# Performance work log

Measured on AMD Instinct MI355X. Metric: run time of the kernel, lower is better.

The kernel has to match this reference:

```python
import jax, jax.numpy as jnp
import numpy as np

HEADS = 4
KS = 7  # neighborhood window size


def group_norm(x, g, b, eps=1e-5):
    # GroupNorm(1, C) on NCHW: normalize over (C,H,W) per sample
    mu = x.mean(axis=(1, 2, 3), keepdims=True)
    var = x.var(axis=(1, 2, 3), keepdims=True)
    xn = (x - mu) * jax.lax.rsqrt(var + eps)
    return xn * g[None, :, None, None] + b[None, :, None, None]


def layer_norm(x, g, b, eps=1e-5):
    mu = x.mean(axis=-1, keepdims=True)
    var = x.var(axis=-1, keepdims=True)
    return (x - mu) * jax.lax.rsqrt(var + eps) * g + b


def na2d(x, qkv_w, qkv_b, proj_w, proj_b, rpb):
    # Neighborhood attention 2D (NATTEN semantics: window clamped at borders)
    N, H, W, C = x.shape
    e, k = HEADS, KS
    d = C // e
    qkv = x @ qkv_w.T + qkv_b  # [N,H,W,3C]
    q, kk, v = jnp.split(qkv, 3, axis=-1)
    q = q.reshape(N, H, W, e, d) * (d ** -0.5)
    kk = kk.reshape(N, H, W, e, d)
    v = v.reshape(N, H, W, e, d)
    ni = jnp.clip(jnp.arange(H) - k // 2, 0, H - k)[:, None] + jnp.arange(k)  # [H,k]
    nj = jnp.clip(jnp.arange(W) - k // 2, 0, W - k)[:, None] + jnp.arange(k)  # [W,k]
    kg = kk[:, ni][:, :, :, nj]  # [N,H,i,W,j,e,d]
    vg = v[:, ni][:, :, :, nj]
    scores = jnp.einsum('nhwed,nhiwjed->nhweij', q, kg)  # [N,H,W,e,k,k]
    ri = ni - jnp.arange(H)[:, None] + (k - 1)  # rel pos index in [0, 2k-2]
    rj = nj - jnp.arange(W)[:, None] + (k - 1)
    bias = rpb[:, ri][:, :, :, rj]  # [e,H,i,W,j]
    scores = scores + bias.transpose(1, 3, 0, 2, 4)[None]
    attn = jax.nn.softmax(scores.reshape(N, H, W, e, k * k), axis=-1).reshape(N, H, W, e, k, k)
    out = jnp.einsum('nhweij,nhiwjed->nhwed', attn, vg).reshape(N, H, W, C)
    return out @ proj_w.T + proj_b


def na_layer(x, gn_g, gn_b, qkv_w, qkv_b, proj_w, proj_b, rpb, ln_g, ln_b, fc1_w, fc1_b, fc2_w, fc2_b):
    N, C, H, W = x.shape
    x1 = x.transpose(0, 2, 3, 1)  # n h w c (pre-norm residual)
    xg = group_norm(x, gn_g, gn_b).transpose(0, 2, 3, 1)
    a = na2d(xg, qkv_w, qkv_b, proj_w, proj_b, rpb) + x1
    t = a.reshape(N, H * W, C)
    h = jax.nn.gelu(layer_norm(t, ln_g, ln_b) @ fc1_w.T + fc1_b, approximate=False)
    t = t + (h @ fc2_w.T + fc2_b)
    return t.reshape(N, H, W, C).transpose(0, 3, 1, 2)


def conv3x3(x, w, b):
    y = jax.lax.conv_general_dilated(x, w, (1, 1), 'SAME', dimension_numbers=('NCHW', 'OIHW', 'NCHW'))
    return y + b[None, :, None, None]


def setup_inputs() -> dict:
    key = jax.random.key(0)
    ks = jax.random.split(key, 16)
    N, C, H, W = 2, 128, 64, 64
    L, e, k, hid, red = 2, HEADS, KS, 4 * 128, 18
    rn = lambda kk, shape, s=0.02: jax.random.normal(kk, shape, jnp.float32) * s
    return {
        'x': jax.random.normal(ks[0], (N, C, H, W), jnp.float32),
        'gn_g': jnp.ones((L, C), jnp.float32), 'gn_b': jnp.zeros((L, C), jnp.float32),
        'qkv_w': rn(ks[1], (L, 3 * C, C)), 'qkv_b': jnp.zeros((L, 3 * C), jnp.float32),
        'proj_w': rn(ks[2], (L, C, C)), 'proj_b': jnp.zeros((L, C), jnp.float32),
        'rpb': rn(ks[3], (L, e, 2 * k - 1, 2 * k - 1)),
        'ln_g': jnp.ones((L, C), jnp.float32), 'ln_b': jnp.zeros((L, C), jnp.float32),
        'fc1_w': rn(ks[4], (L, hid, C)), 'fc1_b': jnp.zeros((L, hid), jnp.float32),
        'fc2_w': rn(ks[5], (L, C, hid)), 'fc2_b': jnp.zeros((L, C), jnp.float32),
        'bconv_w': rn(ks[6], (C, C, 3, 3)), 'bconv_b': jnp.zeros((C,), jnp.float32),
        'c1_w': rn(ks[7], (C // 4, C)), 'c1_b': jnp.zeros((C // 4,), jnp.float32),
        'c2_w': rn(ks[8], (C, C // 4)), 'c2_b': jnp.zeros((C,), jnp.float32),
        'ca1_w': rn(ks[9], (C // red, C)), 'ca1_b': jnp.zeros((C // red,), jnp.float32),
        'ca2_w': rn(ks[10], (C, C // red)), 'ca2_b': jnp.zeros((C,), jnp.float32),
    }


def reference(x, gn_g, gn_b, qkv_w, qkv_b, proj_w, proj_b, rpb, ln_g, ln_b, fc1_w, fc1_b, fc2_w, fc2_b, bconv_w, bconv_b, c1_w, c1_b, c2_w, c2_b, ca1_w, ca1_b, ca2_w, ca2_b):
    res = x
    for l in range(gn_g.shape[0]):  # n_resblocks (structurally fixed, small)
        res = na_layer(res, gn_g[l], gn_b[l], qkv_w[l], qkv_b[l], proj_w[l], proj_b[l], rpb[l],
                       ln_g[l], ln_b[l], fc1_w[l], fc1_b[l], fc2_w[l], fc2_b[l])
    res = conv3x3(res, bconv_w, bconv_b)
    # tail: 1x1 conv -> ReLU -> 1x1 conv -> CALayer
    y = jax.nn.relu(jnp.einsum('rc,nchw->nrhw', c1_w, res) + c1_b[None, :, None, None])
    y = jnp.einsum('cr,nrhw->nchw', c2_w, y) + c2_b[None, :, None, None]
    p = y.mean(axis=(2, 3))  # global avg pool -> [N,C]
    s = jax.nn.sigmoid(jax.nn.relu(p @ ca1_w.T + ca1_b) @ ca2_w.T + ca2_b)
    y = y * s[:, :, None, None]
    return y + x
```

## Files before the change

### kernel.cpp

```cpp
#include <hip/hip_runtime.h>
#include <math.h>

typedef unsigned short u16;

#define NN 2
#define CC 128
#define HH 64
#define WW 64
#define NHD 4
#define DH 32
#define KSZ 7
#define PIX (NN*HH*WW)
#define HID 512
#define C4 32
#define CRED 7
#define RW 22
#define RNB 160
#define NBV 154

typedef float f32x4 __attribute__((ext_vector_type(4)));
typedef short bf16x8 __attribute__((ext_vector_type(8)));

static __device__ __forceinline__ float u2f(u16 u){ return __uint_as_float(((unsigned)u) << 16); }
static __device__ __forceinline__ u16 f2u(float f){
    unsigned b = __float_as_uint(f);
    return (u16)((b + 0x7FFFu + ((b >> 16) & 1u)) >> 16);
}

__global__ void detect_k(const u16* __restrict__ x, int* __restrict__ flag,
                         float* __restrict__ poolacc){
    __shared__ float red[256];
    int t = threadIdx.x;
    float mx = 0.f;
    for(int i = t; i < 4096; i += 256){
        float v = fabsf(u2f(x[i]));
        if(v < 1e30f) mx = fmaxf(mx, v);
    }
    red[t] = mx; __syncthreads();
    for(int s = 128; s > 0; s >>= 1){
        if(t < s) red[t] = fmaxf(red[t], red[t+s]);
        __syncthreads();
    }
    if(t == 0) *flag = (red[0] > 1e6f) ? 1 : 0;
    if(t < NN*CC) poolacc[t] = 0.f;
}

struct PtrTab { const void* p[23]; int off[24]; };
#define NCVT 2172
#define NRPK 576
#define NNCH 512

__global__ __launch_bounds__(256) void setup_k(
    PtrTab tab, u16* __restrict__ Wb, u16* __restrict__ Wt,
    const void* __restrict__ convw, const void* __restrict__ x,
    float* __restrict__ cur, float* __restrict__ part,
    const int* __restrict__ flag, int total)
{
    int blk = blockIdx.x;
    int t = threadIdx.x;
    int fl = *flag;
    if(blk < NCVT){
        int i = blk*256 + t;
        if(i < total){
            int a = 0;
            while(i >= tab.off[a+1]) a++;
            int loc = i - tab.off[a];
            Wb[i] = fl ? f2u(((const float*)tab.p[a])[loc]) : ((const u16*)tab.p[a])[loc];
        }
        return;
    }
    if(blk < NCVT + NRPK){
        int i = (blk - NCVT)*256 + t;
        if(i < CC*CC*9){
            int o = i/(9*CC); int rem = i%(9*CC); int tap = rem/CC; int c = rem%CC;
            size_t s = (size_t)(o*CC + c)*9 + tap;
            Wt[i] = fl ? f2u(((const float*)convw)[s]) : ((const u16*)convw)[s];
        }
        return;
    }
    __shared__ float tile[32][65];
    __shared__ float wred[4][2];
    int u = blk - NCVT - NRPK;
    int bx = u & 3, by = u >> 2;
    int n = by >> 6, i = by & 63;
    for(int idx = t; idx < 32*64; idx += 256){
        int cl = idx >> 6, j = idx & 63;
        size_t src = ((size_t)(n*CC + bx*32 + cl)*HH + i)*WW + j;
        tile[cl][j] = fl ? ((const float*)x)[src] : u2f(((const u16*)x)[src]);
    }
    __syncthreads();
    float s = 0.f, q = 0.f;
    for(int idx = t; idx < 64*32; idx += 256){
        int j = idx >> 5, cl = idx & 31;
        float v = tile[cl][j];
        cur[((size_t)((n*HH + i)*WW) + j)*CC + bx*32 + cl] = v;
        s += v; q += v*v;
    }
    #pragma unroll
    for(int off = 32; off > 0; off >>= 1){ s += __shfl_xor(s, off, 64); q += __shfl_xor(q, off, 64); }
    int wave = t >> 6;
    if((t & 63) == 0){ wred[wave][0] = s; wred[wave][1] = q; }
    __syncthreads();
    if(t == 0){
        float ss = wred[0][0]+wred[1][0]+wred[2][0]+wred[3][0];
        float qq = wred[0][1]+wred[1][1]+wred[2][1]+wred[3][1];
        int pidx = n*256 + i*4 + bx;
        part[pidx*2] = ss; part[pidx*2+1] = qq;
    }
}

enum { EPI_NONE = 0, EPI_RES = 1, EPI_GELU = 2 };
enum { OUT_F32 = 0, OUT_BF16 = 1, OUT_BOTH = 2 };
enum { EX_NONE = 0, EX_STATS = 1 };
#define LDP 136

template<int EPI, int OUTM, int AGN, int EXTRA>
__global__ __launch_bounds__(256) void g64_k(
    const void* __restrict__ Av, const u16* __restrict__ W, const u16* __restrict__ bias,
    const float* __restrict__ R, float* __restrict__ Cf, u16* __restrict__ Cb,
    const u16* __restrict__ gnw, const u16* __restrict__ gnb,
    float* __restrict__ gnpart, int gncount,
    int M, int N, int K)
{
    __shared__ __align__(16) u16 As[64*LDP];
    __shared__ __align__(16) u16 Bs[64*LDP];
    __shared__ float wred[4][2];
    const int bm = blockIdx.y*64, bn = blockIdx.x*64;
    const int t = threadIdx.x;
    const int wave = t >> 6, lane = t & 63;
    const int wm = (wave >> 1)*32, wn = (wave & 1)*32;
    const int lg = lane >> 4, lr = lane & 15;
    const int nsm = bm >> 12;
    f32x4 acc[2][2];
    #pragma unroll
    for(int i = 0; i < 2; i++)
        #pragma unroll
        for(int j = 0; j < 2; j++) acc[i][j] = (f32x4){0.f,0.f,0.f,0.f};

    float gmu = 0.f, grs = 0.f;
    if(AGN){
        float a = 0.f, q = 0.f;
        for(int idx = lane; idx < gncount; idx += 64){
            a += gnpart[(nsm*gncount + idx)*2];
            q += gnpart[(nsm*gncount + idx)*2 + 1];
        }
        #pragma unroll
        for(int off = 32; off > 0; off >>= 1){
            a += __shfl_xor(a, off, 64); q += __shfl_xor(q, off, 64);
        }
        const float inv = 1.f/(float)(HH*WW*CC);
        gmu = a*inv;
        grs = rsqrtf(fmaxf(q*inv - gmu*gmu, 0.f) + 1e-5f);
    }

    for(int k0 = 0; k0 < K; k0 += 128){
        uint4 ra[4], rb[4];
        float4 fa[4][2];
        #pragma unroll
        for(int r = 0; r < 4; r++){
            int e = r*256 + t;
            int row = e >> 4, ch = e & 15;
            if(AGN){
                const float* ap = (const float*)Av + (size_t)(bm+row)*K + k0 + ch*8;
                fa[r][0] = *(const float4*)ap;
                fa[r][1] = *(const float4*)(ap + 4);
            } else {
                ra[r] = *(const uint4*)((const u16*)Av + (size_t)(bm+row)*K + k0 + ch*8);
            }
            rb[r] = (bn+row < N) ? *(const uint4*)(W + (size_t)(bn+row)*K + k0 + ch*8)
                                 : (uint4){0,0,0,0};
        }
        #pragma unroll
        for(int r = 0; r < 4; r++){
            int e = r*256 + t;
            int row = e >> 4, ch = e & 15;
            if(AGN){
                union { uint4 u; u16 h[8]; } g8, b8, o8;
                g8.u = *(const uint4*)(gnw + k0 + ch*8);
                b8.u = *(const uint4*)(gnb + k0 + ch*8);
                const float* fv = (const float*)&fa[r][0];
                #pragma unroll
                for(int z = 0; z < 8; z++)
                    o8.h[z] = f2u((fv[z]-gmu)*grs*u2f(g8.h[z]) + u2f(b8.h[z]));
                *(uint4*)&As[row*LDP + ch*8] = o8.u;
            } else {
                *(uint4*)&As[row*LDP + ch*8] = ra[r];
            }
            *(uint4*)&Bs[row*LDP + ch*8] = rb[r];
        }
        __syncthreads();
        #pragma unroll
        for(int kc = 0; kc < 4; kc++){
            bf16x8 af0 = *(const bf16x8*)&As[(wm + lr)*LDP      + kc*32 + lg*8];
            bf16x8 af1 = *(const bf16x8*)&As[(wm + 16 + lr)*LDP + kc*32 + lg*8];
            bf16x8 bf0 = *(const bf16x8*)&Bs[(wn + lr)*LDP      + kc*32 + lg*8];
            bf16x8 bf1 = *(const bf16x8*)&Bs[(wn + 16 + lr)*LDP + kc*32 + lg*8];
            acc[0][0] = __builtin_amdgcn_mfma_f32_16x16x32_bf16(af0, bf0, acc[0][0], 0, 0, 0);
            acc[0][1] = __builtin_amdgcn_mfma_f32_16x16x32_bf16(af0, bf1, acc[0][1], 0, 0, 0);
            acc[1][0] = __builtin_amdgcn_mfma_f32_16x16x32_bf16(af1, bf0, acc[1][0], 0, 0, 0);
            acc[1][1] = __builtin_amdgcn_mfma_f32_16x16x32_bf16(af1, bf1, acc[1][1], 0, 0, 0);
        }
        if(k0 + 128 < K) __syncthreads();
    }

    float ssum = 0.f, sq = 0.f;
    #pragma unroll
    for(int i = 0; i < 2; i++){
        #pragma unroll
        for(int j = 0; j < 2; j++){
            int col = bn + wn + j*16 + lr;
            if(col >= N) continue;
            #pragma unroll
            for(int reg = 0; reg < 4; reg++){
                int row = bm + wm + i*16 + lg*4 + reg;
                float v = acc[i][j][reg] + u2f(bias[col]);
                if(EPI == EPI_RES)  v += R[(size_t)row*N + col];
                if(EPI == EPI_GELU) v = 0.5f*v*(1.f + erff(v*0.70710678118f));
                if(OUTM == OUT_F32 || OUTM == OUT_BOTH) Cf[(size_t)row*N + col] = v;
                if(OUTM == OUT_BF16 || OUTM == OUT_BOTH) Cb[(size_t)row*N + col] = f2u(v);
                if(EXTRA == EX_STATS){ ssum += v; sq += v*v; }
            }
        }
    }
    if(EXTRA == EX_STATS){
        #pragma unroll
        for(int off = 32; off > 0; off >>= 1){
            ssum += __shfl_xor(ssum, off, 64); sq += __shfl_xor(sq, off, 64);
        }
        if(lane == 0){ wred[wave][0] = ssum; wred[wave][1] = sq; }
        __syncthreads();
        if(t == 0){
            int bidx = blockIdx.y*gridDim.x + blockIdx.x;
            gnpart[bidx*2]   = wred[0][0]+wred[1][0]+wred[2][0]+wred[3][0];
            gnpart[bidx*2+1] = wred[0][1]+wred[1][1]+wred[2][1]+wred[3][1];
        }
    }
}

__global__ __launch_bounds__(256) void proj_ln_k(
    const u16* __restrict__ A, const u16* __restrict__ W, const u16* __restrict__ bias,
    const float* __restrict__ R, const u16* __restrict__ lng, const u16* __restrict__ lnb,
    float* __restrict__ abuf, u16* __restrict__ lnout)
{
    __shared__ __align__(16) u16 As[64*LDP];
    __shared__ __align__(16) u16 Bs[128*LDP];
    __shared__ float redS[64][2], redQ[64][2], muS[64], rsS[64];
    const int bm = blockIdx.x*64;
    const int t = threadIdx.x;
    const int wave = t >> 6, lane = t & 63;
    const int wm = (wave >> 1)*32, wn = (wave & 1)*64;
    const int lg = lane >> 4, lr = lane & 15;

    {
        uint4 ra[4], rb[8];
        #pragma unroll
        for(int r = 0; r < 4; r++){
            int e = r*256 + t; int row = e >> 4, ch = e & 15;
            ra[r] = *(const uint4*)(A + (size_t)(bm+row)*CC + ch*8);
        }
        #pragma unroll
        for(int r = 0; r < 8; r++){
            int e = r*256 + t; int row = e >> 4, ch = e & 15;
            rb[r] = *(const uint4*)(W + (size_t)row*CC + ch*8);
        }
        #pragma unroll
        for(int r = 0; r < 4; r++){
            int e = r*256 + t; int row = e >> 4, ch = e & 15;
            *(uint4*)&As[row*LDP + ch*8] = ra[r];
        }
        #pragma unroll
        for(int r = 0; r < 8; r++){
            int e = r*256 + t; int row = e >> 4, ch = e & 15;
            *(uint4*)&Bs[row*LDP + ch*8] = rb[r];
        }
    }
    __syncthreads();

    f32x4 acc[2][4];
    #pragma unroll
    for(int i = 0; i < 2; i++)
        #pragma unroll
        for(int j = 0; j < 4; j++) acc[i][j] = (f32x4){0.f,0.f,0.f,0.f};
    #pragma unroll
    for(int kc = 0; kc < 4; kc++){
        bf16x8 af[2], bf[4];
        #pragma unroll
        for(int i = 0; i < 2; i++)
            af[i] = *(const bf16x8*)&As[(wm + i*16 + lr)*LDP + kc*32 + lg*8];
        #pragma unroll
        for(int j = 0; j < 4; j++)
            bf[j] = *(const bf16x8*)&Bs[(wn + j*16 + lr)*LDP + kc*32 + lg*8];
        #pragma unroll
        for(int i = 0; i < 2; i++)
            #pragma unroll
            for(int j = 0; j < 4; j++)
                acc[i][j] = __builtin_amdgcn_mfma_f32_16x16x32_bf16(af[i], bf[j], acc[i][j], 0, 0, 0);
    }
    #pragma unroll
    for(int i = 0; i < 2; i++){
        #pragma unroll
        for(int reg = 0; reg < 4; reg++){
            int rl = wm + i*16 + lg*4 + reg;
            float rs_ = 0.f, rq_ = 0.f;
            #pragma unroll
            for(int j = 0; j < 4; j++){
                int col = wn + j*16 + lr;
                float v = acc[i][j][reg] + u2f(bias[col]) + R[(size_t)(bm+rl)*CC + col];
                acc[i][j][reg] = v;
                abuf[(size_t)(bm+rl)*CC + col] = v;
                rs_ += v; rq_ += v*v;
            }
            rs_ += __shfl_xor(rs_, 1, 64); rq_ += __shfl_xor(rq_, 1, 64);
            rs_ += __shfl_xor(rs_, 2, 64); rq_ += __shfl_xor(rq_, 2, 64);
            rs_ += __shfl_xor(rs_, 4, 64); rq_ += __shfl_xor(rq_, 4, 64);
            rs_ += __shfl_xor(rs_, 8, 64); rq_ += __shfl_xor(rq_, 8, 64);
            if(lr == 0){ redS[rl][wn>>6] = rs_; redQ[rl][wn>>6] = rq_; }
        }
    }
    __syncthreads();
    if(t < 64){
        float mu = (redS[t][0] + redS[t][1])*(1.f/CC);
        float var = fmaxf((redQ[t][0] + redQ[t][1])*(1.f/CC) - mu*mu, 0.f);
        muS[t] = mu; rsS[t] = rsqrtf(var + 1e-5f);
    }
    __syncthreads();
    #pragma unroll
    for(int i = 0; i < 2; i++){
        #pragma unroll
        for(int reg = 0; reg < 4; reg++){
            int rl = wm + i*16 + lg*4 + reg;
            float mu = muS[rl], rstd = rsS[rl];
            #pragma unroll
            for(int j = 0; j < 4; j++){
                int col = wn + j*16 + lr;
                float v = (acc[i][j][reg] - mu)*rstd*u2f(lng[col]) + u2f(lnb[col]);
                lnout[(size_t)(bm+rl)*CC + col] = f2u(v);
            }
        }
    }
}

__global__ __launch_bounds__(256) void mconv_k(
    const u16* __restrict__ in, const u16* __restrict__ Wt,
    const u16* __restrict__ bias, u16* __restrict__ Cb)
{
    __shared__ __align__(16) u16 As[64*LDP];
    __shared__ __align__(16) u16 Bs[64*LDP];
    const int bm = blockIdx.y*64, bn = blockIdx.x*64;
    const int t = threadIdx.x;
    const int wave = t >> 6, lane = t & 63;
    const int wm = (wave >> 1)*32, wn = (wave & 1)*32;
    const int lg = lane >> 4, lr = lane & 15;
    f32x4 acc[2][2];
    #pragma unroll
    for(int i = 0; i < 2; i++)
        #pragma unroll
        for(int j = 0; j < 2; j++) acc[i][j] = (f32x4){0.f,0.f,0.f,0.f};

    for(int tap = 0; tap < 9; tap++){
        int dy = tap/3 - 1, dx = tap%3 - 1;
        int k0 = tap*128;
        uint4 ra[4], rb[4];
        #pragma unroll
        for(int r = 0; r < 4; r++){
            int e = r*256 + t;
            int row = e >> 4, ch = e & 15;
            int p = bm + row;
            int n = p >> 12, ii = (p & 4095) >> 6, jj = p & 63;
            int y = ii + dy, x = jj + dx;
            ra[r] = (uint4){0,0,0,0};
            if(y >= 0 && y < HH && x >= 0 && x < WW)
                ra[r] = *(const uint4*)(in + (size_t)(((n*HH + y)*WW + x))*CC + ch*8);
            rb[r] = *(const uint4*)(Wt + (size_t)(bn+row)*(9*CC) + k0 + ch*8);
        }
        #pragma unroll
        for(int r = 0; r < 4; r++){
            int e = r*256 + t;
            int row = e >> 4, ch = e & 15;
            *(uint4*)&As[row*LDP + ch*8] = ra[r];
            *(uint4*)&Bs[row*LDP + ch*8] = rb[r];
        }
        __syncthreads();
        #pragma unroll
        for(int kc = 0; kc < 4; kc++){
            bf16x8 af0 = *(const bf16x8*)&As[(wm + lr)*LDP      + kc*32 + lg*8];
            bf16x8 af1 = *(const bf16x8*)&As[(wm + 16 + lr)*LDP + kc*32 + lg*8];
            bf16x8 bf0 = *(const bf16x8*)&Bs[(wn + lr)*LDP      + kc*32 + lg*8];
            bf16x8 bf1 = *(const bf16x8*)&Bs[(wn + 16 + lr)*LDP + kc*32 + lg*8];
            acc[0][0] = __builtin_amdgcn_mfma_f32_16x16x32_bf16(af0, bf0, acc[0][0], 0, 0, 0);
            acc[0][1] = __builtin_amdgcn_mfma_f32_16x16x32_bf16(af0, bf1, acc[0][1], 0, 0, 0);
            acc[1][0] = __builtin_amdgcn_mfma_f32_16x16x32_bf16(af1, bf0, acc[1][0], 0, 0, 0);
            acc[1][1] = __builtin_amdgcn_mfma_f32_16x16x32_bf16(af1, bf1, acc[1][1], 0, 0, 0);
        }
        if(tap < 8) __syncthreads();
    }
    #pragma unroll
    for(int i = 0; i < 2; i++){
        #pragma unroll
        for(int j = 0; j < 2; j++){
            int col = bn + wn + j*16 + lr;
            #pragma unroll
            for(int reg = 0; reg < 4; reg++){
                int row = bm + wm + i*16 + lg*4 + reg;
                Cb[(size_t)row*CC + col] = f2u(acc[i][j][reg] + u2f(bias[col]));
            }
        }
    }
}

#define KVP 72
#define PSP 168

__global__ __launch_bounds__(128) void att_tile_k(
    const u16* __restrict__ qkv, const u16* __restrict__ rpb, u16* __restrict__ out)
{
    __shared__ __align__(16) u16 KV[2][RNB][KVP];
    __shared__ __align__(16) u16 Qs[16][64];
    __shared__ __align__(16) u16 Ps[2][16][PSP];
    __shared__ float rpbs[2][169];
    const int blk = blockIdx.x;
    const int rb = blk >> 1, eg = blk & 1;
    const int p0 = rb*16;
    const int jb = p0 & 63, i = (p0 >> 6) & 63, n = p0 >> 12;
    const int i0 = min(max(i-3, 0), HH-KSZ);
    const int rc0 = min(max(jb-3, 0), WW-KSZ);
    const int t = threadIdx.x;

    for(int idx = t; idx < 2*169; idx += 128)
        rpbs[idx/169][idx%169] = u2f(rpb[(eg*2 + idx/169)*169 + idx%169]);
    {
        int pix = t >> 3, ch = t & 7;
        *(uint4*)&Qs[pix][ch*8] = *(const uint4*)(qkv + (size_t)(p0+pix)*(3*CC) + eg*64 + ch*8);
    }
    for(int idx = t; idx < RNB*16; idx += 128){
        int nb = idx >> 4, part = idx & 15;
        int kv = part >> 3, ch = part & 7;
        uint4 v = (uint4){0,0,0,0};
        if(nb < NBV){
            int ky = nb/RW, kcol = nb - ky*RW;
            int sy = i0 + ky, sx = min(rc0 + kcol, WW-1);
            v = *(const uint4*)(qkv + (size_t)((n*HH + sy)*WW + sx)*(3*CC) + CC + kv*CC + eg*64 + ch*8);
        }
        *(uint4*)&KV[kv][nb][ch*8] = v;
    }
    __syncthreads();

    const int el = t >> 6;
    const int lane = t & 63, lg = lane >> 4, lr = lane & 15;

    bf16x8 aq = *(const bf16x8*)&Qs[lr][el*32 + lg*8];
    f32x4 sc[10];
    #pragma unroll
    for(int c = 0; c < 10; c++){
        bf16x8 bk = *(const bf16x8*)&KV[0][c*16+lr][el*32 + lg*8];
        sc[c] = __builtin_amdgcn_mfma_f32_16x16x32_bf16(aq, bk, (f32x4){0.f,0.f,0.f,0.f}, 0, 0, 0);
    }
    #pragma unroll
    for(int reg = 0; reg < 4; reg++){
        int pix = lg*4 + reg;
        int j = jb + pix;
        int base = min(max(j-3, 0), WW-KSZ) - rc0;
        float mx = -1e30f;
        #pragma unroll
        for(int c = 0; c < 10; c++){
            int nb = c*16 + lr;
            int ky = nb/RW, kcol = nb - ky*RW;
            float v = -1e30f;
            if(nb < NBV && kcol >= base && kcol <= base+6){
                int ri = i0 + ky - i + (KSZ-1);
                int rj = rc0 + kcol - j + (KSZ-1);
                v = sc[c][reg]*0.17677669529663689f + rpbs[el][ri*13 + rj];
            }
            sc[c][reg] = v;
            mx = fmaxf(mx, v);
        }
        mx = fmaxf(mx, __shfl_xor(mx, 1, 64));
        mx = fmaxf(mx, __shfl_xor(mx, 2, 64));
        mx = fmaxf(mx, __shfl_xor(mx, 4, 64));
        mx = fmaxf(mx, __shfl_xor(mx, 8, 64));
        float sum = 0.f;
        #pragma unroll
        for(int c = 0; c < 10; c++){
            float p = __expf(sc[c][reg] - mx);
            sc[c][reg] = p; sum += p;
        }
        sum += __shfl_xor(sum, 1, 64);
        sum += __shfl_xor(sum, 2, 64);
        sum += __shfl_xor(sum, 4, 64);
        sum += __shfl_xor(sum, 8, 64);
        float rs = 1.f/sum;
        #pragma unroll
        for(int c = 0; c < 10; c++)
            Ps[el][pix][c*16+lr] = f2u(sc[c][reg]*rs);
    }
    __syncthreads();
    f32x4 o0 = (f32x4){0.f,0.f,0.f,0.f}, o1 = (f32x4){0.f,0.f,0.f,0.f};
    #pragma unroll
    for(int ks = 0; ks < 5; ks++){
        bf16x8 ap = *(const bf16x8*)&Ps[el][lr][ks*32 + lg*8];
        bf16x8 b0, b1;
        #pragma unroll
        for(int jj = 0; jj < 8; jj++){
            int nb = ks*32 + lg*8 + jj;
            b0[jj] = (short)KV[1][nb][el*32 + lr];
            b1[jj] = (short)KV[1][nb][el*32 + 16 + lr];
        }
        o0 = __builtin_amdgcn_mfma_f32_16x16x32_bf16(ap, b0, o0, 0, 0, 0);
        o1 = __builtin_amdgcn_mfma_f32_16x16x32_bf16(ap, b1, o1, 0, 0, 0);
    }
    int e = eg*2 + el;
    #pragma unroll
    for(int reg = 0; reg < 4; reg++){
        int pix = lg*4 + reg;
        out[(size_t)(p0+pix)*CC + e*32 + lr]      = f2u(o0[reg]);
        out[(size_t)(p0+pix)*CC + e*32 + 16 + lr] = f2u(o1[reg]);
    }
}

__global__ __launch_bounds__(256) void tail_k(
    const u16* __restrict__ A, const u16* __restrict__ c1w, const u16* __restrict__ c1b,
    const u16* __restrict__ c2w, const u16* __restrict__ c2b,
    float* __restrict__ ybuf, float* __restrict__ poolacc)
{
    __shared__ __align__(16) u16 As[64*LDP];
    __shared__ __align__(16) u16 Bs1[32*LDP];
    __shared__ __align__(16) u16 Hs[64*40];
    __shared__ __align__(16) u16 Bs2[128*40];
    const int bm = blockIdx.x*64;
    const int t = threadIdx.x;
    const int wave = t >> 6, lane = t & 63;
    const int lg = lane >> 4, lr = lane & 15;
    const int nsm = bm >> 12;

    {
        uint4 ra[4], rb1[2], rb2[2];
        #pragma unroll
        for(int r = 0; r < 4; r++){
            int e = r*256 + t; int row = e >> 4, ch = e & 15;
            ra[r] = *(const uint4*)(A + (size_t)(bm+row)*CC + ch*8);
        }
        #pragma unroll
        for(int r = 0; r < 2; r++){
            int e = r*256 + t; int row = e >> 4, ch = e & 15;
            rb1[r] = *(const uint4*)(c1w + (size_t)row*CC + ch*8);
        }
        #pragma unroll
        for(int r = 0; r < 2; r++){
            int e = r*256 + t; int row = e >> 2, ch = e & 3;
            rb2[r] = *(const uint4*)(c2w + (size_t)row*C4 + ch*8);
        }
        #pragma unroll
        for(int r = 0; r < 4; r++){
            int e = r*256 + t; int row = e >> 4, ch = e & 15;
            *(uint4*)&As[row*LDP + ch*8] = ra[r];
        }
        #pragma unroll
        for(int r = 0; r < 2; r++){
            int e = r*256 + t; int row = e >> 4, ch = e & 15;
            *(uint4*)&Bs1[row*LDP + ch*8] = rb1[r];
        }
        #pragma unroll
        for(int r = 0; r < 2; r++){
            int e = r*256 + t; int row = e >> 2, ch = e & 3;
            *(uint4*)&Bs2[row*40 + ch*8] = rb2[r];
        }
    }
    __syncthreads();

    {
        const int wm1 = (wave >> 1)*32, wn1 = (wave & 1)*16;
        f32x4 a1[2];
        a1[0] = (f32x4){0.f,0.f,0.f,0.f}; a1[1] = (f32x4){0.f,0.f,0.f,0.f};
        #pragma unroll
        for(int kc = 0; kc < 4; kc++){
            bf16x8 bf = *(const bf16x8*)&Bs1[(wn1 + lr)*LDP + kc*32 + lg*8];
            bf16x8 af0 = *(const bf16x8*)&As[(wm1 + lr)*LDP      + kc*32 + lg*8];
            bf16x8 af1 = *(const bf16x8*)&As[(wm1 + 16 + lr)*LDP + kc*32 + lg*8];
            a1[0] = __builtin_amdgcn_mfma_f32_16x16x32_bf16(af0, bf, a1[0], 0, 0, 0);
            a1[1] = __builtin_amdgcn_mfma_f32_16x16x32_bf16(af1, bf, a1[1], 0, 0, 0);
        }
        #pragma unroll
        for(int i = 0; i < 2; i++){
            #pragma unroll
            for(int reg = 0; reg < 4; reg++){
                int rl = wm1 + i*16 + lg*4 + reg;
                int col = wn1 + lr;
                Hs[rl*40 + col] = f2u(fmaxf(a1[i][reg] + u2f(c1b[col]), 0.f));
            }
        }
    }
    __syncthreads();

    {
        const int wm = (wave >> 1)*32, wn = (wave & 1)*64;
        f32x4 a2[2][4];
        #pragma unroll
        for(int i = 0; i < 2; i++)
            #pragma unroll
            for(int j = 0; j < 4; j++) a2[i][j] = (f32x4){0.f,0.f,0.f,0.f};
        bf16x8 af[2];
        #pragma unroll
        for(int i = 0; i < 2; i++)
            af[i] = *(const bf16x8*)&Hs[(wm + i*16 + lr)*40 + lg*8];
        #pragma unroll
        for(int j = 0; j < 4; j++){
            bf16x8 bf = *(const bf16x8*)&Bs2[(wn + j*16 + lr)*40 + lg*8];
            a2[0][j] = __builtin_amdgcn_mfma_f32_16x16x32_bf16(af[0], bf, a2[0][j], 0, 0, 0);
            a2[1][j] = __builtin_amdgcn_mfma_f32_16x16x32_bf16(af[1], bf, a2[1][j], 0, 0, 0);
        }
        float cs[4] = {0.f,0.f,0.f,0.f};
        #pragma unroll
        for(int i = 0; i < 2; i++){
            #pragma unroll
            for(int j = 0; j < 4; j++){
                int col = wn + j*16 + lr;
                #pragma unroll
                for(int reg = 0; reg < 4; reg++){
                    int row = bm + wm + i*16 + lg*4 + reg;
                    float v = a2[i][j][reg] + u2f(c2b[col]);
                    ybuf[(size_t)row*CC + col] = v;
                    cs[j] += v;
                }
            }
        }
        #pragma unroll
        for(int j = 0; j < 4; j++){
            cs[j] += __shfl_xor(cs[j], 16, 64);
            cs[j] += __shfl_xor(cs[j], 32, 64);
        }
        if(lg == 0){
            #pragma unroll
            for(int j = 0; j < 4; j++)
                atomicAdd(&poolacc[nsm*CC + wn + j*16 + lr], cs[j]);
        }
    }
}

__global__ __launch_bounds__(256) void final_ca_k(
    const float* __restrict__ y, const float* __restrict__ poolacc,
    const u16* __restrict__ w1, const u16* __restrict__ b1,
    const u16* __restrict__ w2, const u16* __restrict__ b2,
    const void* __restrict__ xraw, void* __restrict__ outv,
    const int* __restrict__ flag)
{
    __shared__ float t1s[CRED];
    __shared__ float sres;
    int id0 = blockIdx.x*256;
    int c = (id0 >> 12) & (CC-1);
    int n = id0 >> 19;
    int t = threadIdx.x;
    if(t < CRED){
        float a = u2f(b1[t]);
        const float pscale = 1.f/(float)(HH*WW);
        for(int cc = 0; cc < CC; cc++)
            a += poolacc[n*CC + cc]*pscale*u2f(w1[t*CC + cc]);
        t1s[t] = fmaxf(a, 0.f);
    }
    __syncthreads();
    if(t == 0){
        float a = u2f(b2[c]);
        #pragma unroll
        for(int r = 0; r < CRED; r++) a += t1s[r]*u2f(w2[c*CRED + r]);
        sres = 1.f/(1.f + __expf(-a));
    }
    __syncthreads();
    float s = sres;
    int id = id0 + t;
    int j = id & 63; int i = (id >> 6) & 63;
    float xr = (*flag) ? ((const float*)xraw)[id] : u2f(((const u16*)xraw)[id]);
    float v = y[(size_t)((n*HH + i)*WW + j)*CC + c]*s + xr;
    if(*flag) ((float*)outv)[id] = v;
    else      ((u16*)outv)[id] = f2u(v);
}

extern "C" void kernel_launch(void* const* d_in, const int* in_sizes, int n_in,
                              void* d_out, int out_size, void* d_ws, size_t ws_size,
                              hipStream_t stream){
    float* wsf    = (float*)d_ws;
    int*   flagp  = (int*)d_ws;
    float* gnpart = wsf + 8;
    float* poolacc= wsf + 1040;

    u16* Wb = (u16*)(wsf + 2048);
    static const int wsizes[23] = {256,256,98304,768,32768,256,1352,256,256,131072,1024,
                                   131072,256,147456,128,4096,32,4096,128,896,7,896,128};
    int woff[24]; woff[0] = 0;
    for(int i = 0; i < 23; i++) woff[i+1] = woff[i] + wsizes[i];
    const int WTOT = woff[23];
    u16* Wt = Wb + 555760;

    float* AB    = wsf + 360448;
    float* cur   = AB;
    u16*  cur16  = (u16*)(AB + 1048576);
    u16*  xg16   = (u16*)(AB + 1572864);
    u16*  qkv16  = (u16*)(AB + 2097152);
    float* abuf  = AB + 2097152;
    u16*  hbuf16 = (u16*)(AB + 3670016);
    float* ybuf  = AB + 3670016;

    detect_k<<<1, 256, 0, stream>>>((const u16*)d_in[0], flagp, poolacc);

    PtrTab tab;
    for(int i = 0; i < 23; i++){ tab.p[i] = d_in[i+1]; tab.off[i] = woff[i]; }
    tab.off[23] = woff[23];
    setup_k<<<NCVT + NRPK + NNCH, 256, 0, stream>>>(
        tab, Wb, Wt, d_in[14], d_in[0], cur, gnpart, flagp, WTOT);

    const u16 *gng = Wb+woff[0], *gnb = Wb+woff[1], *qkvw = Wb+woff[2], *qkvb = Wb+woff[3],
              *projw = Wb+woff[4], *projb = Wb+woff[5], *rpbw = Wb+woff[6], *lng = Wb+woff[7],
              *lnb = Wb+woff[8], *f1w = Wb+woff[9], *f1b = Wb+woff[10], *f2w = Wb+woff[11],
              *f2b = Wb+woff[12], *bcb = Wb+woff[14], *c1w = Wb+woff[15],
              *c1b = Wb+woff[16], *c2w = Wb+woff[17], *c2b = Wb+woff[18], *ca1w = Wb+woff[19],
              *ca1b = Wb+woff[20], *ca2w = Wb+woff[21], *ca2b = Wb+woff[22];

    for(int l = 0; l < 2; l++){
        int gncount = (l == 0) ? 256 : 128;

        g64_k<EPI_NONE,OUT_BF16,1,EX_NONE><<<dim3(6, PIX/64), 256, 0, stream>>>(
            cur, qkvw + (size_t)l*3*CC*CC, qkvb + l*3*CC, nullptr, nullptr, qkv16,
            gng + l*CC, gnb + l*CC, gnpart, gncount, PIX, 3*CC, CC);

        att_tile_k<<<PIX/16*2, 128, 0, stream>>>(qkv16, rpbw + l*NHD*169, xg16);

        proj_ln_k<<<PIX/64, 256, 0, stream>>>(
            xg16, projw + (size_t)l*CC*CC, projb + l*CC, cur, lng + l*CC, lnb + l*CC,
            abuf, xg16);

        g64_k<EPI_GELU,OUT_BF16,0,EX_NONE><<<dim3(8, PIX/64), 256, 0, stream>>>(
            xg16, f1w + (size_t)l*HID*CC, f1b + l*HID, nullptr, nullptr, hbuf16,
            nullptr, nullptr, nullptr, 0, PIX, HID, CC);

        g64_k<EPI_RES,OUT_BOTH,0,EX_STATS><<<dim3(2, PIX/64), 256, 0, stream>>>(
            hbuf16, f2w + (size_t)l*CC*HID, f2b + l*CC, abuf, cur, cur16,
            nullptr, nullptr, gnpart, 0, PIX, CC, HID);
    }

    mconv_k<<<dim3(2, PIX/64), 256, 0, stream>>>(cur16, Wt, bcb, xg16);

    tail_k<<<PIX/64, 256, 0, stream>>>(xg16, c1w, c1b, c2w, c2b, ybuf, poolacc);

    final_ca_k<<<(NN*CC*HH*WW)/256, 256, 0, stream>>>(
        ybuf, poolacc, ca1w, ca1b, ca2w, ca2b, d_in[0], d_out, flagp);
}
```

Before: 268.9 us.

## Fuse 3x3 conv with tail 1x1 convs and shrink proj_ln tiles to 32 rows

```diff
diff --git a/kernel.cpp b/kernel.cpp
--- a/kernel.cpp
+++ b/kernel.cpp
@@ -242,19 +242,19 @@
     const float* __restrict__ R, const u16* __restrict__ lng, const u16* __restrict__ lnb,
     float* __restrict__ abuf, u16* __restrict__ lnout)
 {
-    __shared__ __align__(16) u16 As[64*LDP];
+    __shared__ __align__(16) u16 As[32*LDP];
     __shared__ __align__(16) u16 Bs[128*LDP];
-    __shared__ float redS[64][2], redQ[64][2], muS[64], rsS[64];
-    const int bm = blockIdx.x*64;
+    __shared__ float redS[32][2], redQ[32][2], muS[32], rsS[32];
+    const int bm = blockIdx.x*32;
     const int t = threadIdx.x;
     const int wave = t >> 6, lane = t & 63;
-    const int wm = (wave >> 1)*32, wn = (wave & 1)*64;
+    const int wm = (wave >> 1)*16, wn = (wave & 1)*64;
     const int lg = lane >> 4, lr = lane & 15;
 
     {
-        uint4 ra[4], rb[8];
-        #pragma unroll
-        for(int r = 0; r < 4; r++){
+        uint4 ra[2], rb[8];
+        #pragma unroll
+        for(int r = 0; r < 2; r++){
             int e = r*256 + t; int row = e >> 4, ch = e & 15;
             ra[r] = *(const uint4*)(A + (size_t)(bm+row)*CC + ch*8);
         }
@@ -264,7 +264,7 @@
             rb[r] = *(const uint4*)(W + (size_t)row*CC + ch*8);
         }
         #pragma unroll
-        for(int r = 0; r < 4; r++){
+        for(int r = 0; r < 2; r++){
             int e = r*256 + t; int row = e >> 4, ch = e & 15;
             *(uint4*)&As[row*LDP + ch*8] = ra[r];
         }
@@ -276,134 +276,201 @@
     }
     __syncthreads();
 
-    f32x4 acc[2][4];
-    #pragma unroll
-    for(int i = 0; i < 2; i++)
-        #pragma unroll
-        for(int j = 0; j < 4; j++) acc[i][j] = (f32x4){0.f,0.f,0.f,0.f};
+    f32x4 acc[4];
+    #pragma unroll
+    for(int j = 0; j < 4; j++) acc[j] = (f32x4){0.f,0.f,0.f,0.f};
     #pragma unroll
     for(int kc = 0; kc < 4; kc++){
-        bf16x8 af[2], bf[4];
-        #pragma unroll
-        for(int i = 0; i < 2; i++)
-            af[i] = *(const bf16x8*)&As[(wm + i*16 + lr)*LDP + kc*32 + lg*8];
-        #pragma unroll
-        for(int j = 0; j < 4; j++)
-            bf[j] = *(const bf16x8*)&Bs[(wn + j*16 + lr)*LDP + kc*32 + lg*8];
-        #pragma unroll
-        for(int i = 0; i < 2; i++)
-            #pragma unroll
-            for(int j = 0; j < 4; j++)
-                acc[i][j] = __builtin_amdgcn_mfma_f32_16x16x32_bf16(af[i], bf[j], acc[i][j], 0, 0, 0);
-    }
-    #pragma unroll
-    for(int i = 0; i < 2; i++){
-        #pragma unroll
-        for(int reg = 0; reg < 4; reg++){
-            int rl = wm + i*16 + lg*4 + reg;
-            float rs_ = 0.f, rq_ = 0.f;
-            #pragma unroll
-            for(int j = 0; j < 4; j++){
-                int col = wn + j*16 + lr;
-                float v = acc[i][j][reg] + u2f(bias[col]) + R[(size_t)(bm+rl)*CC + col];
-                acc[i][j][reg] = v;
-                abuf[(size_t)(bm+rl)*CC + col] = v;
-                rs_ += v; rq_ += v*v;
-            }
-            rs_ += __shfl_xor(rs_, 1, 64); rq_ += __shfl_xor(rq_, 1, 64);
-            rs_ += __shfl_xor(rs_, 2, 64); rq_ += __shfl_xor(rq_, 2, 64);
-            rs_ += __shfl_xor(rs_, 4, 64); rq_ += __shfl_xor(rq_, 4, 64);
-            rs_ += __shfl_xor(rs_, 8, 64); rq_ += __shfl_xor(rq_, 8, 64);
-            if(lr == 0){ redS[rl][wn>>6] = rs_; redQ[rl][wn>>6] = rq_; }
-        }
-    }
-    __syncthreads();
-    if(t < 64){
+        bf16x8 af = *(const bf16x8*)&As[(wm + lr)*LDP + kc*32 + lg*8];
+        #pragma unroll
+        for(int j = 0; j < 4; j++){
+            bf16x8 bf = *(const bf16x8*)&Bs[(wn + j*16 + lr)*LDP + kc*32 + lg*8];
+            acc[j] = __builtin_amdgcn_mfma_f32_16x16x32_bf16(af, bf, acc[j], 0, 0, 0);
+        }
+    }
+    #pragma unroll
+    for(int reg = 0; reg < 4; reg++){
+        int rl = wm + lg*4 + reg;
+        float rs_ = 0.f, rq_ = 0.f;
+        #pragma unroll
+        for(int j = 0; j < 4; j++){
+            int col = wn + j*16 + lr;
+            float v = acc[j][reg] + u2f(bias[col]) + R[(size_t)(bm+rl)*CC + col];
+            acc[j][reg] = v;
+            abuf[(size_t)(bm+rl)*CC + col] = v;
+            rs_ += v; rq_ += v*v;
+        }
+        rs_ += __shfl_xor(rs_, 1, 64); rq_ += __shfl_xor(rq_, 1, 64);
+        rs_ += __shfl_xor(rs_, 2, 64); rq_ += __shfl_xor(rq_, 2, 64);
+        rs_ += __shfl_xor(rs_, 4, 64); rq_ += __shfl_xor(rq_, 4, 64);
+        rs_ += __shfl_xor(rs_, 8, 64); rq_ += __shfl_xor(rq_, 8, 64);
+        if(lr == 0){ redS[rl][wn>>6] = rs_; redQ[rl][wn>>6] = rq_; }
+    }
+    __syncthreads();
+    if(t < 32){
         float mu = (redS[t][0] + redS[t][1])*(1.f/CC);
         float var = fmaxf((redQ[t][0] + redQ[t][1])*(1.f/CC) - mu*mu, 0.f);
         muS[t] = mu; rsS[t] = rsqrtf(var + 1e-5f);
     }
     __syncthreads();
     #pragma unroll
-    for(int i = 0; i < 2; i++){
-        #pragma unroll
-        for(int reg = 0; reg < 4; reg++){
-            int rl = wm + i*16 + lg*4 + reg;
-            float mu = muS[rl], rstd = rsS[rl];
-            #pragma unroll
-            for(int j = 0; j < 4; j++){
-                int col = wn + j*16 + lr;
-                float v = (acc[i][j][reg] - mu)*rstd*u2f(lng[col]) + u2f(lnb[col]);
-                lnout[(size_t)(bm+rl)*CC + col] = f2u(v);
-            }
-        }
-    }
-}
-
-__global__ __launch_bounds__(256) void mconv_k(
-    const u16* __restrict__ in, const u16* __restrict__ Wt,
-    const u16* __restrict__ bias, u16* __restrict__ Cb)
+    for(int reg = 0; reg < 4; reg++){
+        int rl = wm + lg*4 + reg;
+        float mu = muS[rl], rstd = rsS[rl];
+        #pragma unroll
+        for(int j = 0; j < 4; j++){
+            int col = wn + j*16 + lr;
+            float v = (acc[j][reg] - mu)*rstd*u2f(lng[col]) + u2f(lnb[col]);
+            lnout[(size_t)(bm+rl)*CC + col] = f2u(v);
+        }
+    }
+}
+
+__global__ __launch_bounds__(256) void mct_k(
+    const u16* __restrict__ in, const u16* __restrict__ Wt, const u16* __restrict__ bias,
+    const u16* __restrict__ c1w, const u16* __restrict__ c1b,
+    const u16* __restrict__ c2w, const u16* __restrict__ c2b,
+    float* __restrict__ ybuf, float* __restrict__ poolacc)
 {
-    __shared__ __align__(16) u16 As[64*LDP];
-    __shared__ __align__(16) u16 Bs[64*LDP];
-    const int bm = blockIdx.y*64, bn = blockIdx.x*64;
+    __shared__ __align__(16) u16 As[32*LDP];
+    __shared__ __align__(16) u16 Bs[128*LDP];
+    u16* Bs1 = Bs;
+    u16* Bs2 = Bs + 32*LDP;
+    u16* Hs  = Bs + 32*LDP + 128*40;
+    const int bm = blockIdx.x*32;
     const int t = threadIdx.x;
     const int wave = t >> 6, lane = t & 63;
-    const int wm = (wave >> 1)*32, wn = (wave & 1)*32;
+    const int wm = (wave >> 1)*16, wn = (wave & 1)*64;
     const int lg = lane >> 4, lr = lane & 15;
-    f32x4 acc[2][2];
-    #pragma unroll
-    for(int i = 0; i < 2; i++)
-        #pragma unroll
-        for(int j = 0; j < 2; j++) acc[i][j] = (f32x4){0.f,0.f,0.f,0.f};
+    const int nsm = bm >> 12;
+
+    uint4 rb1[2], rb2[2];
+    #pragma unroll
+    for(int r = 0; r < 2; r++){
+        int e = r*256 + t; int row = e >> 4, ch = e & 15;
+        rb1[r] = *(const uint4*)(c1w + (size_t)row*CC + ch*8);
+    }
+    #pragma unroll
+    for(int r = 0; r < 2; r++){
+        int e = r*256 + t; int row = e >> 2, ch = e & 3;
+        rb2[r] = *(const uint4*)(c2w + (size_t)row*C4 + ch*8);
+    }
+
+    f32x4 acc[4];
+    #pragma unroll
+    for(int j = 0; j < 4; j++) acc[j] = (f32x4){0.f,0.f,0.f,0.f};
 
     for(int tap = 0; tap < 9; tap++){
         int dy = tap/3 - 1, dx = tap%3 - 1;
-        int k0 = tap*128;
-        uint4 ra[4], rb[4];
-        #pragma unroll
-        for(int r = 0; r < 4; r++){
-            int e = r*256 + t;
-            int row = e >> 4, ch = e & 15;
+        uint4 ra[2], rb[8];
+        #pragma unroll
+        for(int r = 0; r < 2; r++){
+            int e = r*256 + t; int row = e >> 4, ch = e & 15;
             int p = bm + row;
             int n = p >> 12, ii = (p & 4095) >> 6, jj = p & 63;
             int y = ii + dy, x = jj + dx;
             ra[r] = (uint4){0,0,0,0};
             if(y >= 0 && y < HH && x >= 0 && x < WW)
                 ra[r] = *(const uint4*)(in + (size_t)(((n*HH + y)*WW + x))*CC + ch*8);
-            rb[r] = *(const uint4*)(Wt + (size_t)(bn+row)*(9*CC) + k0 + ch*8);
-        }
-        #pragma unroll
-        for(int r = 0; r < 4; r++){
-            int e = r*256 + t;
-            int row = e >> 4, ch = e & 15;
+        }
+        #pragma unroll
+        for(int r = 0; r < 8; r++){
+            int e = r*256 + t; int row = e >> 4, ch = e & 15;
+            rb[r] = *(const uint4*)(Wt + (size_t)row*(9*CC) + tap*128 + ch*8);
+        }
+        #pragma unroll
+        for(int r = 0; r < 2; r++){
+            int e = r*256 + t; int row = e >> 4, ch = e & 15;
             *(uint4*)&As[row*LDP + ch*8] = ra[r];
+        }
+        #pragma unroll
+        for(int r = 0; r < 8; r++){
+            int e = r*256 + t; int row = e >> 4, ch = e & 15;
             *(uint4*)&Bs[row*LDP + ch*8] = rb[r];
         }
         __syncthreads();
         #pragma unroll
         for(int kc = 0; kc < 4; kc++){
-            bf16x8 af0 = *(const bf16x8*)&As[(wm + lr)*LDP      + kc*32 + lg*8];
-            bf16x8 af1 = *(const bf16x8*)&As[(wm + 16 + lr)*LDP + kc*32 + lg*8];
-            bf16x8 bf0 = *(const bf16x8*)&Bs[(wn + lr)*LDP      + kc*32 + lg*8];
-            bf16x8 bf1 = *(const bf16x8*)&Bs[(wn + 16 + lr)*LDP + kc*32 + lg*8];
-            acc[0][0] = __builtin_amdgcn_mfma_f32_16x16x32_bf16(af0, bf0, acc[0][0], 0, 0, 0);
-            acc[0][1] = __builtin_amdgcn_mfma_f32_16x16x32_bf16(af0, bf1, acc[0][1], 0, 0, 0);
-            acc[1][0] = __builtin_amdgcn_mfma_f32_16x16x32_bf16(af1, bf0, acc[1][0], 0, 0, 0);
-            acc[1][1] = __builtin_amdgcn_mfma_f32_16x16x32_bf16(af1, bf1, acc[1][1], 0, 0, 0);
-        }
-        if(tap < 8) __syncthreads();
-    }
-    #pragma unroll
-    for(int i = 0; i < 2; i++){
-        #pragma unroll
-        for(int j = 0; j < 2; j++){
-            int col = bn + wn + j*16 + lr;
+            bf16x8 af = *(const bf16x8*)&As[(wm + lr)*LDP + kc*32 + lg*8];
+            #pragma unroll
+            for(int j = 0; j < 4; j++){
+                bf16x8 bf = *(const bf16x8*)&Bs[(wn + j*16 + lr)*LDP + kc*32 + lg*8];
+                acc[j] = __builtin_amdgcn_mfma_f32_16x16x32_bf16(af, bf, acc[j], 0, 0, 0);
+            }
+        }
+        __syncthreads();
+    }
+
+    #pragma unroll
+    for(int j = 0; j < 4; j++){
+        int col = wn + j*16 + lr;
+        #pragma unroll
+        for(int reg = 0; reg < 4; reg++){
+            int rl = wm + lg*4 + reg;
+            As[rl*LDP + col] = f2u(acc[j][reg] + u2f(bias[col]));
+        }
+    }
+    #pragma unroll
+    for(int r = 0; r < 2; r++){
+        int e = r*256 + t; int row = e >> 4, ch = e & 15;
+        *(uint4*)&Bs1[row*LDP + ch*8] = rb1[r];
+    }
+    #pragma unroll
+    for(int r = 0; r < 2; r++){
+        int e = r*256 + t; int row = e >> 2, ch = e & 3;
+        *(uint4*)&Bs2[row*40 + ch*8] = rb2[r];
+    }
+    __syncthreads();
+
+    {
+        const int wn1 = (wave & 1)*16;
+        f32x4 a1 = (f32x4){0.f,0.f,0.f,0.f};
+        #pragma unroll
+        for(int kc = 0; kc < 4; kc++){
+            bf16x8 af = *(const bf16x8*)&As[(wm + lr)*LDP + kc*32 + lg*8];
+            bf16x8 bf = *(const bf16x8*)&Bs1[(wn1 + lr)*LDP + kc*32 + lg*8];
+            a1 = __builtin_amdgcn_mfma_f32_16x16x32_bf16(af, bf, a1, 0, 0, 0);
+        }
+        #pragma unroll
+        for(int reg = 0; reg < 4; reg++){
+            int rl = wm + lg*4 + reg;
+            int col = wn1 + lr;
+            Hs[rl*40 + col] = f2u(fmaxf(a1[reg] + u2f(c1b[col]), 0.f));
+        }
+    }
+    __syncthreads();
+
+    {
+        f32x4 a2[4];
+        #pragma unroll
+        for(int j = 0; j < 4; j++) a2[j] = (f32x4){0.f,0.f,0.f,0.f};
+        bf16x8 af = *(const bf16x8*)&Hs[(wm + lr)*40 + lg*8];
+        #pragma unroll
+        for(int j = 0; j < 4; j++){
+            bf16x8 bf = *(const bf16x8*)&Bs2[(wn + j*16 + lr)*40 + lg*8];
+            a2[j] = __builtin_amdgcn_mfma_f32_16x16x32_bf16(af, bf, a2[j], 0, 0, 0);
+        }
+        float cs[4] = {0.f,0.f,0.f,0.f};
+        #pragma unroll
+        for(int j = 0; j < 4; j++){
+            int col = wn + j*16 + lr;
             #pragma unroll
             for(int reg = 0; reg < 4; reg++){
-                int row = bm + wm + i*16 + lg*4 + reg;
-                Cb[(size_t)row*CC + col] = f2u(acc[i][j][reg] + u2f(bias[col]));
+                int row = bm + wm + lg*4 + reg;
+                float v = a2[j][reg] + u2f(c2b[col]);
+                ybuf[(size_t)row*CC + col] = v;
+                cs[j] += v;
             }
+        }
+        #pragma unroll
+        for(int j = 0; j < 4; j++){
+            cs[j] += __shfl_xor(cs[j], 16, 64);
+            cs[j] += __shfl_xor(cs[j], 32, 64);
+        }
+        if(lg == 0){
+            #pragma unroll
+            for(int j = 0; j < 4; j++)
+                atomicAdd(&poolacc[nsm*CC + wn + j*16 + lr], cs[j]);
         }
     }
 }
@@ -416,8 +483,8 @@
 {
     __shared__ __align__(16) u16 KV[2][RNB][KVP];
     __shared__ __align__(16) u16 Qs[16][64];
-    __shared__ __align__(16) u16 Ps[2][16][PSP];
     __shared__ float rpbs[2][169];
+    u16* PsB = &KV[0][0][0];
     const int blk = blockIdx.x;
     const int rb = blk >> 1, eg = blk & 1;
     const int p0 = rb*16;
@@ -455,6 +522,7 @@
         bf16x8 bk = *(const bf16x8*)&KV[0][c*16+lr][el*32 + lg*8];
         sc[c] = __builtin_amdgcn_mfma_f32_16x16x32_bf16(aq, bk, (f32x4){0.f,0.f,0.f,0.f}, 0, 0, 0);
     }
+    __syncthreads();
     #pragma unroll
     for(int reg = 0; reg < 4; reg++){
         int pix = lg*4 + reg;
@@ -491,13 +559,13 @@
         float rs = 1.f/sum;
         #pragma unroll
         for(int c = 0; c < 10; c++)
-            Ps[el][pix][c*16+lr] = f2u(sc[c][reg]*rs);
+            PsB[(el*16 + pix)*PSP + c*16 + lr] = f2u(sc[c][reg]*rs);
     }
     __syncthreads();
     f32x4 o0 = (f32x4){0.f,0.f,0.f,0.f}, o1 = (f32x4){0.f,0.f,0.f,0.f};
     #pragma unroll
     for(int ks = 0; ks < 5; ks++){
-        bf16x8 ap = *(const bf16x8*)&Ps[el][lr][ks*32 + lg*8];
+        bf16x8 ap = *(const bf16x8*)&PsB[(el*16 + lr)*PSP + ks*32 + lg*8];
         bf16x8 b0, b1;
         #pragma unroll
         for(int jj = 0; jj < 8; jj++){
@@ -514,125 +582,6 @@
         int pix = lg*4 + reg;
         out[(size_t)(p0+pix)*CC + e*32 + lr]      = f2u(o0[reg]);
         out[(size_t)(p0+pix)*CC + e*32 + 16 + lr] = f2u(o1[reg]);
-    }
-}
-
-__global__ __launch_bounds__(256) void tail_k(
-    const u16* __restrict__ A, const u16* __restrict__ c1w, const u16* __restrict__ c1b,
-    const u16* __restrict__ c2w, const u16* __restrict__ c2b,
-    float* __restrict__ ybuf, float* __restrict__ poolacc)
-{
-    __shared__ __align__(16) u16 As[64*LDP];
-    __shared__ __align__(16) u16 Bs1[32*LDP];
-    __shared__ __align__(16) u16 Hs[64*40];
-    __shared__ __align__(16) u16 Bs2[128*40];
-    const int bm = blockIdx.x*64;
-    const int t = threadIdx.x;
-    const int wave = t >> 6, lane = t & 63;
-    const int lg = lane >> 4, lr = lane & 15;
-    const int nsm = bm >> 12;
-
-    {
-        uint4 ra[4], rb1[2], rb2[2];
-        #pragma unroll
-        for(int r = 0; r < 4; r++){
-            int e = r*256 + t; int row = e >> 4, ch = e & 15;
-            ra[r] = *(const uint4*)(A + (size_t)(bm+row)*CC + ch*8);
-        }
-        #pragma unroll
-        for(int r = 0; r < 2; r++){
-            int e = r*256 + t; int row = e >> 4, ch = e & 15;
-            rb1[r] = *(const uint4*)(c1w + (size_t)row*CC + ch*8);
-        }
-        #pragma unroll
-        for(int r = 0; r < 2; r++){
-            int e = r*256 + t; int row = e >> 2, ch = e & 3;
-            rb2[r] = *(const uint4*)(c2w + (size_t)row*C4 + ch*8);
-        }
-        #pragma unroll
-        for(int r = 0; r < 4; r++){
-            int e = r*256 + t; int row = e >> 4, ch = e & 15;
-            *(uint4*)&As[row*LDP + ch*8] = ra[r];
-        }
-        #pragma unroll
-        for(int r = 0; r < 2; r++){
-            int e = r*256 + t; int row = e >> 4, ch = e & 15;
-            *(uint4*)&Bs1[row*LDP + ch*8] = rb1[r];
-        }
-        #pragma unroll
-        for(int r = 0; r < 2; r++){
-            int e = r*256 + t; int row = e >> 2, ch = e & 3;
-            *(uint4*)&Bs2[row*40 + ch*8] = rb2[r];
-        }
-    }
-    __syncthreads();
-
-    {
-        const int wm1 = (wave >> 1)*32, wn1 = (wave & 1)*16;
-        f32x4 a1[2];
-        a1[0] = (f32x4){0.f,0.f,0.f,0.f}; a1[1] = (f32x4){0.f,0.f,0.f,0.f};
-        #pragma unroll
-        for(int kc = 0; kc < 4; kc++){
-            bf16x8 bf = *(const bf16x8*)&Bs1[(wn1 + lr)*LDP + kc*32 + lg*8];
-            bf16x8 af0 = *(const bf16x8*)&As[(wm1 + lr)*LDP      + kc*32 + lg*8];
-            bf16x8 af1 = *(const bf16x8*)&As[(wm1 + 16 + lr)*LDP + kc*32 + lg*8];
-            a1[0] = __builtin_amdgcn_mfma_f32_16x16x32_bf16(af0, bf, a1[0], 0, 0, 0);
-            a1[1] = __builtin_amdgcn_mfma_f32_16x16x32_bf16(af1, bf, a1[1], 0, 0, 0);
-        }
-        #pragma unroll
-        for(int i = 0; i < 2; i++){
-            #pragma unroll
-            for(int reg = 0; reg < 4; reg++){
-                int rl = wm1 + i*16 + lg*4 + reg;
-                int col = wn1 + lr;
-                Hs[rl*40 + col] = f2u(fmaxf(a1[i][reg] + u2f(c1b[col]), 0.f));
-            }
-        }
-    }
-    __syncthreads();
-
-    {
-        const int wm = (wave >> 1)*32, wn = (wave & 1)*64;
-        f32x4 a2[2][4];
-        #pragma unroll
-        for(int i = 0; i < 2; i++)
-            #pragma unroll
-            for(int j = 0; j < 4; j++) a2[i][j] = (f32x4){0.f,0.f,0.f,0.f};
-        bf16x8 af[2];
-        #pragma unroll
-        for(int i = 0; i < 2; i++)
-            af[i] = *(const bf16x8*)&Hs[(wm + i*16 + lr)*40 + lg*8];
-        #pragma unroll
-        for(int j = 0; j < 4; j++){
-            bf16x8 bf = *(const bf16x8*)&Bs2[(wn + j*16 + lr)*40 + lg*8];
-            a2[0][j] = __builtin_amdgcn_mfma_f32_16x16x32_bf16(af[0], bf, a2[0][j], 0, 0, 0);
-            a2[1][j] = __builtin_amdgcn_mfma_f32_16x16x32_bf16(af[1], bf, a2[1][j], 0, 0, 0);
-        }
-        float cs[4] = {0.f,0.f,0.f,0.f};
-        #pragma unroll
-        for(int i = 0; i < 2; i++){
-            #pragma unroll
-            for(int j = 0; j < 4; j++){
-                int col = wn + j*16 + lr;
-                #pragma unroll
-                for(int reg = 0; reg < 4; reg++){
-                    int row = bm + wm + i*16 + lg*4 + reg;
-                    float v = a2[i][j][reg] + u2f(c2b[col]);
-                    ybuf[(size_t)row*CC + col] = v;
-                    cs[j] += v;
-                }
-            }
-        }
-        #pragma unroll
-        for(int j = 0; j < 4; j++){
-            cs[j] += __shfl_xor(cs[j], 16, 64);
-            cs[j] += __shfl_xor(cs[j], 32, 64);
-        }
-        if(lg == 0){
-            #pragma unroll
-            for(int j = 0; j < 4; j++)
-                atomicAdd(&poolacc[nsm*CC + wn + j*16 + lr], cs[j]);
-        }
     }
 }
 
@@ -722,7 +671,7 @@
 
         att_tile_k<<<PIX/16*2, 128, 0, stream>>>(qkv16, rpbw + l*NHD*169, xg16);
 
-        proj_ln_k<<<PIX/64, 256, 0, stream>>>(
+        proj_ln_k<<<PIX/32, 256, 0, stream>>>(
             xg16, projw + (size_t)l*CC*CC, projb + l*CC, cur, lng + l*CC, lnb + l*CC,
             abuf, xg16);
 
@@ -735,9 +684,7 @@
             nullptr, nullptr, gnpart, 0, PIX, CC, HID);
     }
 
-    mconv_k<<<dim3(2, PIX/64), 256, 0, stream>>>(cur16, Wt, bcb, xg16);
-
-    tail_k<<<PIX/64, 256, 0, stream>>>(xg16, c1w, c1b, c2w, c2b, ybuf, poolacc);
+    mct_k<<<PIX/32, 256, 0, stream>>>(cur16, Wt, bcb, c1w, c1b, c2w, c2b, ybuf, poolacc);
 
     final_ca_k<<<(NN*CC*HH*WW)/256, 256, 0, stream>>>(
         ybuf, poolacc, ca1w, ca1b, ca2w, ca2b, d_in[0], d_out, flagp);
```

New measurement: 271.8 us. About the same (+1.1%).
